# Performance work log

Measured on AMD Instinct MI355X. Metric: run time of the kernel, lower is better.

Reference implementation:

```python
import jax, jax.numpy as jnp
import numpy as np

B, T, C = 2, 2048, 1024
H = 16
HS = C // H  # 64

def setup_inputs() -> dict:
    key = jax.random.key(0)
    ks = jax.random.split(key, 5)
    s = 0.02  # typical init scale for stability
    return {
        "x": jax.random.normal(ks[0], (B, T, C), dtype=jnp.float32),
        "Wq": jax.random.normal(ks[1], (C, C), dtype=jnp.float32) * s,
        "Wk": jax.random.normal(ks[2], (C, C), dtype=jnp.float32) * s,
        "Wv": jax.random.normal(ks[3], (C, C), dtype=jnp.float32) * s,
        "Wp": jax.random.normal(ks[4], (C, C), dtype=jnp.float32) * s,
    }

def reference(x, Wq, Wk, Wv, Wp):
    b, t, c = x.shape
    # nn.Linear(bias=False): y = x @ W.T
    q = (x @ Wq.T).reshape(b, t, H, HS).transpose(0, 2, 1, 3)  # [b,h,t,hs]
    k = (x @ Wk.T).reshape(b, t, H, HS).transpose(0, 2, 1, 3)
    v = (x @ Wv.T).reshape(b, t, H, HS).transpose(0, 2, 1, 3)
    att = jnp.einsum('bhqd,bhkd->bhqk', q, k) / jnp.sqrt(jnp.float32(HS))
    # quirk: masked_fill with 0 (NOT -inf) on the strict upper triangle, then softmax
    mask = jnp.triu(jnp.ones((t, t), dtype=bool), k=1)
    att = jnp.where(mask, 0.0, att)
    att = jax.nn.softmax(att, axis=-1)
    y = jnp.einsum('bhqk,bhkd->bhqd', att, v)  # [b,h,t,hs]
    y = y.transpose(0, 2, 1, 3).reshape(b, t, c)
    return y @ Wp.T
```

## Files before the change

### kernel.cpp

```cpp
#include <hip/hip_runtime.h>
#include <hip/hip_bf16.h>
#include <math.h>

#define BB 2
#define TT 2048
#define CC 1024
#define HH 16
#define HS 64
#define NROWS (BB * TT)
#define QTILES (TT / 64)

typedef __attribute__((ext_vector_type(8))) short short8v;
typedef __attribute__((ext_vector_type(4))) float f32x4;
typedef __attribute__((ext_vector_type(4))) unsigned int u32x4;
typedef unsigned short u16;

__device__ __forceinline__ u16 f2bf(float f) {
    return __builtin_bit_cast(u16, (__bf16)f);
}

__device__ __forceinline__ void glds16(const void* g, void* l) {
    __builtin_amdgcn_global_load_lds((__attribute__((address_space(1))) void*)g,
                                     (__attribute__((address_space(3))) void*)l, 16, 0, 0);
}
#define WAITV(N) asm volatile("s_waitcnt vmcnt(" #N ")" ::: "memory")
#define BAR() do { __builtin_amdgcn_s_barrier(); __builtin_amdgcn_sched_barrier(0); } while (0)

__device__ __forceinline__ void swap32(unsigned& a, unsigned& b) {
    asm volatile("v_permlane32_swap_b32 %0, %1" : "+v"(a), "+v"(b));
}
__device__ __forceinline__ void swap16(unsigned& a, unsigned& b) {
    asm volatile("v_permlane16_swap_b32 %0, %1" : "+v"(a), "+v"(b));
}

__global__ __launch_bounds__(256) void fsplit_kernel(const float* __restrict__ x,
                                                     const float* __restrict__ Wq, const float* __restrict__ Wk,
                                                     const float* __restrict__ Wv, const float* __restrict__ Wp,
                                                     u16* __restrict__ xh,
                                                     u16* __restrict__ wqk,
                                                     u16* __restrict__ wv, u16* __restrict__ wp) {
    const size_t WC = (size_t)CC * CC;
    const int bid = blockIdx.x;
    const float* src; u16* dh; float sc = 1.f; int i;
    if (bid < 4096) {
        src = x; dh = xh; i = bid * 256 + threadIdx.x;
    } else {
        const int wsel = (bid - 4096) >> 10;
        i = ((bid - 4096) & 1023) * 256 + threadIdx.x;
        if (wsel == 0)      { src = Wq; dh = wqk;      sc = 0.125f * 1.4426950408889634f; }
        else if (wsel == 1) { src = Wk; dh = wqk + WC; }
        else if (wsel == 2) { src = Wv; dh = wv; }
        else                { src = Wp; dh = wp; }
    }
    float4 v = ((const float4*)src)[i];
    v.x *= sc; v.y *= sc; v.z *= sc; v.w *= sc;
    ushort4 H;
    H.x = f2bf(v.x); H.y = f2bf(v.y); H.z = f2bf(v.z); H.w = f2bf(v.w);
    ((ushort4*)dh)[i] = H;
}

__global__ __launch_bounds__(256) void qkv_kernel(const u16* __restrict__ xh, const u16* __restrict__ wqk,
                                                  const u16* __restrict__ wv,
                                                  u16* __restrict__ Qo, u16* __restrict__ Ko,
                                                  u16* __restrict__ VtO, float* __restrict__ TSg) {
    __shared__ u16 lA[2 * 4096], lB[2 * 4096];
    const int tid = threadIdx.x;
    const int lane = tid & 63, w = tid >> 6;
    const int wr = w >> 1, wc = w & 1;
    const int fr = lane & 15, fc = lane >> 4;
    const int K = CC;

    const int gbid = blockIdx.x;
    const bool isQK = gbid < 512;
    const int sub = isQK ? gbid : gbid - 512;
    const int nbx = isQK ? 16 : 32;
    const int nwg = isQK ? 512 : 256;
    const u16* __restrict__ A = isQK ? xh : wv;
    const u16* __restrict__ B = isQK ? wqk : xh;

    const int swz = (sub & 7) * (nwg >> 3) + (sub >> 3);
    const int bm = (swz / nbx) * 128, bn = (swz % nbx) * 128;

    f32x4 acc[4][4];
    #pragma unroll
    for (int i = 0; i < 4; ++i)
        #pragma unroll
        for (int j = 0; j < 4; ++j) acc[i][j] = (f32x4){0.f, 0.f, 0.f, 0.f};

    const int lrow = lane >> 2, lcs = lane & 3;
    const int rA0 = w * 16 + lrow, rA1 = rA0 + 64;
    const size_t aoff0 = (size_t)(bm + rA0) * K + (lcs ^ ((rA0 >> 1) & 3)) * 8;
    const size_t aoff1 = (size_t)(bm + rA1) * K + (lcs ^ ((rA1 >> 1) & 3)) * 8;
    const size_t boff0 = (size_t)(bn + rA0) * K + (lcs ^ ((rA0 >> 1) & 3)) * 8;
    const size_t boff1 = (size_t)(bn + rA1) * K + (lcs ^ ((rA1 >> 1) & 3)) * 8;
    const int d0 = w * 512, d1 = 2048 + w * 512;

    int aslot[4], bslot[4];
    #pragma unroll
    for (int mi = 0; mi < 4; ++mi) {
        int row = wr * 64 + mi * 16 + fr;
        aslot[mi] = row * 4 + (fc ^ ((row >> 1) & 3));
    }
    #pragma unroll
    for (int ni = 0; ni < 4; ++ni) {
        int col = wc * 64 + ni * 16 + fr;
        bslot[ni] = col * 4 + (fc ^ ((col >> 1) & 3));
    }

    auto STAGE = [&](int t, int buf) {
        const int k0 = t * 32;
        const int bo = buf * 4096;
        glds16(A + aoff0 + k0, lA + bo + d0);
        glds16(A + aoff1 + k0, lA + bo + d1);
        glds16(B + boff0 + k0, lB + bo + d0);
        glds16(B + boff1 + k0, lB + bo + d1);
    };

    const int nt = K >> 5;
    STAGE(0, 0);

    #pragma unroll 2
    for (int t = 0; t < nt; ++t) {
        const int cur = t & 1;
        BAR();
        if (t + 1 < nt) { STAGE(t + 1, cur ^ 1); WAITV(4); }
        else            { WAITV(0); }

        const int co = cur * 512;
        short8v fa[4], fb[4];
        #pragma unroll
        for (int mi = 0; mi < 4; ++mi) fa[mi] = ((const short8v*)lA)[co + aslot[mi]];
        #pragma unroll
        for (int ni = 0; ni < 4; ++ni) fb[ni] = ((const short8v*)lB)[co + bslot[ni]];
        __builtin_amdgcn_s_setprio(1);
        #pragma unroll
        for (int mi = 0; mi < 4; ++mi)
            #pragma unroll
            for (int ni = 0; ni < 4; ++ni)
                acc[mi][ni] = __builtin_amdgcn_mfma_f32_16x16x32_bf16(fa[mi], fb[ni], acc[mi][ni], 0, 0, 0);
        __builtin_amdgcn_s_setprio(0);
    }

    const int fq = lane >> 4;
    if (isQK) {
        #pragma unroll
        for (int mi = 0; mi < 4; ++mi)
            #pragma unroll
            for (int ni = 0; ni < 4; ++ni)
                #pragma unroll
                for (int r = 0; r < 4; ++r) {
                    const int rg = bm + wr * 64 + mi * 16 + fq * 4 + r;
                    const int cg = bn + wc * 64 + ni * 16 + fr;
                    const u16 hh = f2bf(acc[mi][ni][r]);
                    if (cg < CC) Qo[(size_t)rg * CC + cg] = hh;
                    else         Ko[(size_t)rg * CC + cg - CC] = hh;
                }
    } else {
        #pragma unroll
        for (int mi = 0; mi < 4; ++mi)
            #pragma unroll
            for (int ni = 0; ni < 4; ++ni)
                #pragma unroll
                for (int r = 0; r < 4; ++r) {
                    const int rg = bm + wr * 64 + mi * 16 + fq * 4 + r;
                    const int cg = bn + wc * 64 + ni * 16 + fr;
                    const int bq = cg >> 11, tq = cg & 2047;
                    const int hq = rg >> 6, dq = rg & 63;
                    VtO[((size_t)((bq << 4) + hq) * HS + dq) * TT + tq] = f2bf(acc[mi][ni][r]);
                }
        __syncthreads();
        float* TSL = (float*)lA;
        #pragma unroll
        for (int mi = 0; mi < 4; ++mi)
            #pragma unroll
            for (int r = 0; r < 4; ++r) {
                float s = acc[mi][0][r] + acc[mi][1][r] + acc[mi][2][r] + acc[mi][3][r];
                s += __shfl_xor(s, 1); s += __shfl_xor(s, 2);
                s += __shfl_xor(s, 4); s += __shfl_xor(s, 8);
                if (fr == 0) TSL[wc * 128 + wr * 64 + mi * 16 + fq * 4 + r] = s;
            }
        __syncthreads();
        {
            const int wcq = tid >> 7, row = tid & 127;
            const int col0 = bn + wcq * 64;
            const int bq = col0 >> 11, qtv = (col0 & 2047) >> 6;
            const int bhh = (bq << 4) + ((bm + row) >> 6);
            const int dq = (bm + row) & 63;
            TSg[((size_t)bhh * QTILES + qtv) * 64 + dq] = TSL[tid];
        }
    }
}

__global__ __launch_bounds__(64) void scan_kernel(const float* __restrict__ TSg,
                                                  float* __restrict__ STile) {
    const int bh = blockIdx.x;
    const int d = threadIdx.x;
    float s = 0.f;
    STile[((size_t)bh * 33 + 32) * 64 + d] = 0.f;
    for (int qt = QTILES - 1; qt >= 0; --qt) {
        s += TSg[((size_t)bh * QTILES + qt) * 64 + d];
        STile[((size_t)bh * 33 + qt) * 64 + d] = s;
    }
}

__global__ __launch_bounds__(256) void gemm_proj(const u16* __restrict__ A, const u16* __restrict__ B,
                                                 float* __restrict__ O, int M, int N, int K) {
    constexpr int GNT = 64;
    __shared__ u16 lA[2 * 4096], lB[2 * GNT * 32];
    const int tid = threadIdx.x;
    const int lane = tid & 63, w = tid >> 6;
    const int wr = w >> 1, wc = w & 1;
    const int fr = lane & 15, fc = lane >> 4;

    const int nbx = gridDim.x;
    const int bid = blockIdx.y * nbx + blockIdx.x;
    const int nwg = nbx * gridDim.y;
    const int swz = (bid & 7) * (nwg >> 3) + (bid >> 3);
    const int bm = (swz / nbx) * 128, bn = (swz % nbx) * GNT;

    f32x4 acc[4][2];
    #pragma unroll
    for (int i = 0; i < 4; ++i)
        #pragma unroll
        for (int j = 0; j < 2; ++j) acc[i][j] = (f32x4){0.f, 0.f, 0.f, 0.f};

    const int lrow = lane >> 2, lcs = lane & 3;
    const int rA0 = w * 16 + lrow, rA1 = rA0 + 64;
    const size_t aoff0 = (size_t)(bm + rA0) * K + (lcs ^ ((rA0 >> 1) & 3)) * 8;
    const size_t aoff1 = (size_t)(bm + rA1) * K + (lcs ^ ((rA1 >> 1) & 3)) * 8;
    const size_t boff0 = (size_t)(bn + rA0) * K + (lcs ^ ((rA0 >> 1) & 3)) * 8;
    const int d0 = w * 512, d1 = 2048 + w * 512;

    int aslot[4], bslot[2];
    #pragma unroll
    for (int mi = 0; mi < 4; ++mi) {
        int row = wr * 64 + mi * 16 + fr;
        aslot[mi] = row * 4 + (fc ^ ((row >> 1) & 3));
    }
    #pragma unroll
    for (int ni = 0; ni < 2; ++ni) {
        int col = wc * 32 + ni * 16 + fr;
        bslot[ni] = col * 4 + (fc ^ ((col >> 1) & 3));
    }

    auto STAGE = [&](int t, int buf) {
        const int k0 = t * 32;
        const int bo = buf * 4096;
        glds16(A + aoff0 + k0, lA + bo + d0);
        glds16(A + aoff1 + k0, lA + bo + d1);
        const int bo2 = buf * 2048;
        glds16(B + boff0 + k0, lB + bo2 + d0);
    };

    const int nt = K >> 5;
    STAGE(0, 0);

    #pragma unroll 2
    for (int t = 0; t < nt; ++t) {
        const int cur = t & 1;
        BAR();
        if (t + 1 < nt) { STAGE(t + 1, cur ^ 1); WAITV(3); }
        else            { WAITV(0); }

        const int co = cur * 512, co2 = cur * 256;
        short8v fa[4], fb[2];
        #pragma unroll
        for (int mi = 0; mi < 4; ++mi) fa[mi] = ((const short8v*)lA)[co + aslot[mi]];
        #pragma unroll
        for (int ni = 0; ni < 2; ++ni) fb[ni] = ((const short8v*)lB)[co2 + bslot[ni]];
        __builtin_amdgcn_s_setprio(1);
        #pragma unroll
        for (int mi = 0; mi < 4; ++mi)
            #pragma unroll
            for (int ni = 0; ni < 2; ++ni)
                acc[mi][ni] = __builtin_amdgcn_mfma_f32_16x16x32_bf16(fa[mi], fb[ni], acc[mi][ni], 0, 0, 0);
        __builtin_amdgcn_s_setprio(0);
    }

    const int fq = lane >> 4;
    #pragma unroll
    for (int mi = 0; mi < 4; ++mi)
        #pragma unroll
        for (int ni = 0; ni < 2; ++ni)
            #pragma unroll
            for (int r = 0; r < 4; ++r) {
                const int rg = bm + wr * 64 + mi * 16 + fq * 4 + r;
                const int cg = bn + wc * 32 + ni * 16 + fr;
                O[(size_t)rg * N + cg] = acc[mi][ni][r];
            }
}

__global__ __launch_bounds__(256, 4) void attn_kernel(const u16* __restrict__ Qh,
                                                      const u16* __restrict__ Kh,
                                                      const u16* __restrict__ Vt,
                                                      const float* __restrict__ STile,
                                                      u16* __restrict__ Yh) {
    const int g = blockIdx.x;
    const int bh = (g & 7) + 8 * ((g >> 3) & 3);
    const int qt = 31 - (g >> 5);
    const int b = bh >> 4, h = bh & 15;
    const int tid = threadIdx.x;
    const int w = tid >> 6, lane = tid & 63;
    const int lx = lane & 15, hi4 = lane >> 4;

    __shared__ u16 Ksh[2 * 4096];
    __shared__ u16 Vsh[2 * 4096];

    const u16* Kg = Kh + (size_t)b * TT * CC + h * HS;
    const u16* Vg = Vt + (size_t)bh * HS * TT;

    const int s0 = w * 64 + lane, s1 = 256 + w * 64 + lane;
    const int rr0 = s0 >> 3, gc0 = (s0 & 7) ^ (rr0 & 7);
    const int rr1 = s1 >> 3, gc1 = (s1 & 7) ^ (rr1 & 7);
    const int db0 = (w * 64) * 8, db1 = (256 + w * 64) * 8;
    const size_t kbase0 = (size_t)rr0 * CC + gc0 * 8;
    const size_t kbase1 = (size_t)rr1 * CC + gc1 * 8;
    const size_t vbase0 = (size_t)rr0 * TT + gc0 * 8;
    const size_t vbase1 = (size_t)rr1 * TT + gc1 * 8;

    auto stage = [&](int kt, int buf) {
        const size_t ko = (size_t)kt * 64 * CC;
        const int vo = kt * 64;
        const int bo = buf * 4096;
        glds16(Kg + ko + kbase0, Ksh + bo + db0);
        glds16(Kg + ko + kbase1, Ksh + bo + db1);
        glds16(Vg + vbase0 + vo, Vsh + bo + db0);
        glds16(Vg + vbase1 + vo, Vsh + bo + db1);
    };

    short8v nones[2];
    #pragma unroll
    for (int k0 = 0; k0 < 2; ++k0)
        #pragma unroll
        for (int jj = 0; jj < 8; ++jj)
            nones[k0][jj] = (short)(((k0 * 32 + hi4 * 8 + jj) <= (w * 16 + lx)) ? 0xBF80 : 0);

    stage(0, 0);

    const size_t qoff = (size_t)(b * TT + qt * 64 + w * 16 + lx) * CC + h * HS + hi4 * 8;
    short8v qf[2];
    qf[0] = *(const short8v*)(Qh + qoff); qf[1] = *(const short8v*)(Qh + qoff + 32);

    const f32x4 zero = {0.f, 0.f, 0.f, 0.f};
    f32x4 y4[4];
    float lsum = 0.f;
    #pragma unroll
    for (int dt = 0; dt < 4; ++dt) y4[dt] = zero;

    int cur = 0;
    for (int kt = 0; kt <= qt; ++kt) {
        WAITV(0);
        BAR();
        if (kt < qt) stage(kt + 1, cur ^ 1);

        const int co = cur * 512;
        const bool diag = (kt == qt);

        f32x4 s4[4];
        #pragma unroll
        for (int j = 0; j < 4; ++j) s4[j] = zero;
        __builtin_amdgcn_s_setprio(1);
        #pragma unroll
        for (int j = 0; j < 4; ++j) {
            const int keyr = j * 16 + lx;
            const int rb = keyr * 8, sw = keyr & 7;
            #pragma unroll
            for (int d0 = 0; d0 < 2; ++d0) {
                const short8v kb = ((const short8v*)Ksh)[co + rb + ((hi4 + 4 * d0) ^ sw)];
                s4[j] = __builtin_amdgcn_mfma_f32_16x16x32_bf16(kb, qf[d0], s4[j], 0, 0, 0);
            }
        }
        __builtin_amdgcn_s_setprio(0);

        unsigned Wpk[4][2];
        #pragma unroll
        for (int j = 0; j < 4; ++j) {
            float pv[4];
            #pragma unroll
            for (int r = 0; r < 4; ++r) {
                float e = __builtin_amdgcn_exp2f(s4[j][r]);
                if (diag && (j * 16 + hi4 * 4 + r) > (w * 16 + lx)) e = 0.f;
                lsum += e;
                pv[r] = e;
            }
            Wpk[j][0] = (unsigned)f2bf(pv[0]) | ((unsigned)f2bf(pv[1]) << 16);
            Wpk[j][1] = (unsigned)f2bf(pv[2]) | ((unsigned)f2bf(pv[3]) << 16);
        }
        #pragma unroll
        for (int j1 = 0; j1 < 2; ++j1)
            #pragma unroll
            for (int hh = 0; hh < 2; ++hh) {
                swap32(Wpk[2 * j1][hh], Wpk[2 * j1 + 1][hh]);
                swap16(Wpk[2 * j1][hh], Wpk[2 * j1 + 1][hh]);
            }
        short8v pa[2];
        #pragma unroll
        for (int k0 = 0; k0 < 2; ++k0) {
            u32x4 ah = {Wpk[2 * k0][0], Wpk[2 * k0][1], Wpk[2 * k0 + 1][0], Wpk[2 * k0 + 1][1]};
            pa[k0] = __builtin_bit_cast(short8v, ah);
        }

        __builtin_amdgcn_s_setprio(1);
        #pragma unroll
        for (int dt = 0; dt < 4; ++dt) {
            const int drow = dt * 16 + lx;
            const int rb = drow * 8, sw = drow & 7;
            #pragma unroll
            for (int k0 = 0; k0 < 2; ++k0) {
                const short8v vb = ((const short8v*)Vsh)[co + rb + ((hi4 + 4 * k0) ^ sw)];
                y4[dt] = __builtin_amdgcn_mfma_f32_16x16x32_bf16(pa[k0], vb, y4[dt], 0, 0, 0);
                if (diag)
                    y4[dt] = __builtin_amdgcn_mfma_f32_16x16x32_bf16(nones[k0], vb, y4[dt], 0, 0, 0);
            }
        }
        __builtin_amdgcn_s_setprio(0);

        cur ^= 1;
    }

    lsum += __shfl_xor(lsum, 16);
    lsum += __shfl_xor(lsum, 32);
    float l4[4];
    #pragma unroll
    for (int r = 0; r < 4; ++r) l4[r] = __shfl(lsum, hi4 * 4 + r);

    const float* stp = STile + ((size_t)bh * 33 + qt) * 64;
    #pragma unroll
    for (int dt = 0; dt < 4; ++dt) {
        const float st = stp[dt * 16 + lx];
        #pragma unroll
        for (int r = 0; r < 4; ++r) {
            const int t = qt * 64 + w * 16 + hi4 * 4 + r;
            const float linv = 1.f / (l4[r] + (float)(TT - 1 - t));
            const float yv = (y4[dt][r] + st) * linv;
            const size_t off = (size_t)(b * TT + t) * CC + h * HS + dt * 16 + lx;
            Yh[off] = f2bf(yv);
        }
    }
}

extern "C" void kernel_launch(void* const* d_in, const int* in_sizes, int n_in,
                              void* d_out, int out_size, void* d_ws, size_t ws_size,
                              hipStream_t stream) {
    const float* x  = (const float*)d_in[0];
    const float* Wq = (const float*)d_in[1];
    const float* Wk = (const float*)d_in[2];
    const float* Wv = (const float*)d_in[3];
    const float* Wp = (const float*)d_in[4];
    float* out = (float*)d_out;

    char* ws = (char*)d_ws;
    u16* xh = (u16*)ws;
    u16* Yh = xh;
    u16* Qh = (u16*)(ws + (16u << 20));
    u16* Kh = (u16*)(ws + (32u << 20));
    u16* wv = (u16*)(ws + (48u << 20));
    float* TSg = (float*)(ws + (52u << 20));
    u16* wp = (u16*)(ws + (56u << 20));
    float* St = (float*)(ws + (64u << 20));
    u16* wqk = (u16*)out;
    u16* Vth = (u16*)((char*)out + (4u << 20));

    fsplit_kernel<<<8192, 256, 0, stream>>>(x, Wq, Wk, Wv, Wp, xh, wqk, wv, wp);

    qkv_kernel<<<768, 256, 0, stream>>>(xh, wqk, wv, Qh, Kh, Vth, TSg);

    scan_kernel<<<BB * HH, 64, 0, stream>>>(TSg, St);

    attn_kernel<<<1024, 256, 0, stream>>>(Qh, Kh, Vth, St, Yh);

    gemm_proj<<<dim3(CC / 64, NROWS / 128), 256, 0, stream>>>(Yh, wp, out, NROWS, CC, CC);
}
```

Baseline: 104.8 us.

## Fold suffix-sum scan into attention kernel and enlarge projection GEMM tile

Removes the separate scan kernel launch. Each attention block now computes its own suffix sum of the per-tile V sums directly from TSg, using a 4-way split reduction in shared memory, and the first K/V stage is issued before this reduction so the two overlap. Separately, the output projection GEMM tile grows from 128x64 to 128x128, which halves the block count and doubles per-wave MFMA work for better reuse of A. The cost is redundant suffix-sum reads across blocks, and fewer GEMM blocks (256) that may underfill the device.

```diff
diff --git a/kernel.cpp b/kernel.cpp
--- a/kernel.cpp
+++ b/kernel.cpp
@@ -191,22 +191,9 @@
     }
 }
 
-__global__ __launch_bounds__(64) void scan_kernel(const float* __restrict__ TSg,
-                                                  float* __restrict__ STile) {
-    const int bh = blockIdx.x;
-    const int d = threadIdx.x;
-    float s = 0.f;
-    STile[((size_t)bh * 33 + 32) * 64 + d] = 0.f;
-    for (int qt = QTILES - 1; qt >= 0; --qt) {
-        s += TSg[((size_t)bh * QTILES + qt) * 64 + d];
-        STile[((size_t)bh * 33 + qt) * 64 + d] = s;
-    }
-}
-
 __global__ __launch_bounds__(256) void gemm_proj(const u16* __restrict__ A, const u16* __restrict__ B,
                                                  float* __restrict__ O, int M, int N, int K) {
-    constexpr int GNT = 64;
-    __shared__ u16 lA[2 * 4096], lB[2 * GNT * 32];
+    __shared__ u16 lA[2 * 4096], lB[2 * 4096];
     const int tid = threadIdx.x;
     const int lane = tid & 63, w = tid >> 6;
     const int wr = w >> 1, wc = w & 1;
@@ -216,30 +203,31 @@
     const int bid = blockIdx.y * nbx + blockIdx.x;
     const int nwg = nbx * gridDim.y;
     const int swz = (bid & 7) * (nwg >> 3) + (bid >> 3);
-    const int bm = (swz / nbx) * 128, bn = (swz % nbx) * GNT;
-
-    f32x4 acc[4][2];
+    const int bm = (swz / nbx) * 128, bn = (swz % nbx) * 128;
+
+    f32x4 acc[4][4];
     #pragma unroll
     for (int i = 0; i < 4; ++i)
         #pragma unroll
-        for (int j = 0; j < 2; ++j) acc[i][j] = (f32x4){0.f, 0.f, 0.f, 0.f};
+        for (int j = 0; j < 4; ++j) acc[i][j] = (f32x4){0.f, 0.f, 0.f, 0.f};
 
     const int lrow = lane >> 2, lcs = lane & 3;
     const int rA0 = w * 16 + lrow, rA1 = rA0 + 64;
     const size_t aoff0 = (size_t)(bm + rA0) * K + (lcs ^ ((rA0 >> 1) & 3)) * 8;
     const size_t aoff1 = (size_t)(bm + rA1) * K + (lcs ^ ((rA1 >> 1) & 3)) * 8;
     const size_t boff0 = (size_t)(bn + rA0) * K + (lcs ^ ((rA0 >> 1) & 3)) * 8;
+    const size_t boff1 = (size_t)(bn + rA1) * K + (lcs ^ ((rA1 >> 1) & 3)) * 8;
     const int d0 = w * 512, d1 = 2048 + w * 512;
 
-    int aslot[4], bslot[2];
+    int aslot[4], bslot[4];
     #pragma unroll
     for (int mi = 0; mi < 4; ++mi) {
         int row = wr * 64 + mi * 16 + fr;
         aslot[mi] = row * 4 + (fc ^ ((row >> 1) & 3));
     }
     #pragma unroll
-    for (int ni = 0; ni < 2; ++ni) {
-        int col = wc * 32 + ni * 16 + fr;
+    for (int ni = 0; ni < 4; ++ni) {
+        int col = wc * 64 + ni * 16 + fr;
         bslot[ni] = col * 4 + (fc ^ ((col >> 1) & 3));
     }
 
@@ -248,8 +236,8 @@
         const int bo = buf * 4096;
         glds16(A + aoff0 + k0, lA + bo + d0);
         glds16(A + aoff1 + k0, lA + bo + d1);
-        const int bo2 = buf * 2048;
-        glds16(B + boff0 + k0, lB + bo2 + d0);
+        glds16(B + boff0 + k0, lB + bo + d0);
+        glds16(B + boff1 + k0, lB + bo + d1);
     };
 
     const int nt = K >> 5;
@@ -259,20 +247,20 @@
     for (int t = 0; t < nt; ++t) {
         const int cur = t & 1;
         BAR();
-        if (t + 1 < nt) { STAGE(t + 1, cur ^ 1); WAITV(3); }
+        if (t + 1 < nt) { STAGE(t + 1, cur ^ 1); WAITV(4); }
         else            { WAITV(0); }
 
-        const int co = cur * 512, co2 = cur * 256;
-        short8v fa[4], fb[2];
+        const int co = cur * 512;
+        short8v fa[4], fb[4];
         #pragma unroll
         for (int mi = 0; mi < 4; ++mi) fa[mi] = ((const short8v*)lA)[co + aslot[mi]];
         #pragma unroll
-        for (int ni = 0; ni < 2; ++ni) fb[ni] = ((const short8v*)lB)[co2 + bslot[ni]];
+        for (int ni = 0; ni < 4; ++ni) fb[ni] = ((const short8v*)lB)[co + bslot[ni]];
         __builtin_amdgcn_s_setprio(1);
         #pragma unroll
         for (int mi = 0; mi < 4; ++mi)
             #pragma unroll
-            for (int ni = 0; ni < 2; ++ni)
+            for (int ni = 0; ni < 4; ++ni)
                 acc[mi][ni] = __builtin_amdgcn_mfma_f32_16x16x32_bf16(fa[mi], fb[ni], acc[mi][ni], 0, 0, 0);
         __builtin_amdgcn_s_setprio(0);
     }
@@ -281,11 +269,11 @@
     #pragma unroll
     for (int mi = 0; mi < 4; ++mi)
         #pragma unroll
-        for (int ni = 0; ni < 2; ++ni)
+        for (int ni = 0; ni < 4; ++ni)
             #pragma unroll
             for (int r = 0; r < 4; ++r) {
                 const int rg = bm + wr * 64 + mi * 16 + fq * 4 + r;
-                const int cg = bn + wc * 32 + ni * 16 + fr;
+                const int cg = bn + wc * 64 + ni * 16 + fr;
                 O[(size_t)rg * N + cg] = acc[mi][ni][r];
             }
 }
@@ -293,7 +281,7 @@
 __global__ __launch_bounds__(256, 4) void attn_kernel(const u16* __restrict__ Qh,
                                                       const u16* __restrict__ Kh,
                                                       const u16* __restrict__ Vt,
-                                                      const float* __restrict__ STile,
+                                                      const float* __restrict__ TSg,
                                                       u16* __restrict__ Yh) {
     const int g = blockIdx.x;
     const int bh = (g & 7) + 8 * ((g >> 3) & 3);
@@ -305,6 +293,8 @@
 
     __shared__ u16 Ksh[2 * 4096];
     __shared__ u16 Vsh[2 * 4096];
+    __shared__ float stp4[4][64];
+    __shared__ float stS[64];
 
     const u16* Kg = Kh + (size_t)b * TT * CC + h * HS;
     const u16* Vg = Vt + (size_t)bh * HS * TT;
@@ -328,14 +318,25 @@
         glds16(Vg + vbase1 + vo, Vsh + bo + db1);
     };
 
+    stage(0, 0);
+
+    {
+        const int d = tid & 63, grp = tid >> 6;
+        float part = 0.f;
+        for (int t2 = qt + grp; t2 < QTILES; t2 += 4)
+            part += TSg[((size_t)bh * QTILES + t2) * 64 + d];
+        stp4[grp][d] = part;
+        __syncthreads();
+        if (tid < 64) stS[tid] = stp4[0][tid] + stp4[1][tid] + stp4[2][tid] + stp4[3][tid];
+        __syncthreads();
+    }
+
     short8v nones[2];
     #pragma unroll
     for (int k0 = 0; k0 < 2; ++k0)
         #pragma unroll
         for (int jj = 0; jj < 8; ++jj)
             nones[k0][jj] = (short)(((k0 * 32 + hi4 * 8 + jj) <= (w * 16 + lx)) ? 0xBF80 : 0);
-
-    stage(0, 0);
 
     const size_t qoff = (size_t)(b * TT + qt * 64 + w * 16 + lx) * CC + h * HS + hi4 * 8;
     short8v qf[2];
@@ -424,10 +425,9 @@
     #pragma unroll
     for (int r = 0; r < 4; ++r) l4[r] = __shfl(lsum, hi4 * 4 + r);
 
-    const float* stp = STile + ((size_t)bh * 33 + qt) * 64;
     #pragma unroll
     for (int dt = 0; dt < 4; ++dt) {
-        const float st = stp[dt * 16 + lx];
+        const float st = stS[dt * 16 + lx];
         #pragma unroll
         for (int r = 0; r < 4; ++r) {
             const int t = qt * 64 + w * 16 + hi4 * 4 + r;
@@ -457,7 +457,6 @@
     u16* wv = (u16*)(ws + (48u << 20));
     float* TSg = (float*)(ws + (52u << 20));
     u16* wp = (u16*)(ws + (56u << 20));
-    float* St = (float*)(ws + (64u << 20));
     u16* wqk = (u16*)out;
     u16* Vth = (u16*)((char*)out + (4u << 20));
 
@@ -465,9 +464,7 @@
 
     qkv_kernel<<<768, 256, 0, stream>>>(xh, wqk, wv, Qh, Kh, Vth, TSg);
 
-    scan_kernel<<<BB * HH, 64, 0, stream>>>(TSg, St);
-
-    attn_kernel<<<1024, 256, 0, stream>>>(Qh, Kh, Vth, St, Yh);
-
-    gemm_proj<<<dim3(CC / 64, NROWS / 128), 256, 0, stream>>>(Yh, wp, out, NROWS, CC, CC);
-}
+    attn_kernel<<<1024, 256, 0, stream>>>(Qh, Kh, Vth, TSg, Yh);
+
+    gemm_proj<<<dim3(CC / 128, NROWS / 128), 256, 0, stream>>>(Yh, wp, out, NROWS, CC, CC);
+}
```

Result: no change. 104.9 us (+0.1%).
